# Performance work log

Hardware: AMD Instinct MI355X
Metric: run time of the kernel (lower is better)

## Reference

```python
import jax, jax.numpy as jnp
import numpy as np
from math import sqrt

B, T, C = 4, 2048, 2048
H = 16
D = C // H  # head_dim = 128


def setup_inputs() -> dict:
    key = jax.random.key(0)
    ks = jax.random.split(key, 7)
    s = 1.0 / sqrt(C)
    return {
        "querys": jax.random.normal(ks[0], (B, T, C), dtype=jnp.float32),
        "keys": jax.random.normal(ks[1], (B, T, C), dtype=jnp.float32),
        "values": jax.random.normal(ks[2], (B, T, C), dtype=jnp.float32),
        "Wq": jax.random.normal(ks[3], (C, C), dtype=jnp.float32) * s,
        "bq": jnp.zeros((C,), dtype=jnp.float32),
        "Wk": jax.random.normal(ks[4], (C, C), dtype=jnp.float32) * s,
        "bk": jnp.zeros((C,), dtype=jnp.float32),
        "Wv": jax.random.normal(ks[5], (C, C), dtype=jnp.float32) * s,
        "bv": jnp.zeros((C,), dtype=jnp.float32),
        "Wo": jax.random.normal(ks[6], (C, C), dtype=jnp.float32) * s,
        "bo": jnp.zeros((C,), dtype=jnp.float32),
        "is_causal": 1,
    }


def reference(querys, keys, values, Wq, bq, Wk, bk, Wv, bv, Wo, bo, is_causal):
    # Linear projections: x @ W^T + b (torch nn.Linear convention), here W stored as [C_in, C_out]
    q = (querys @ Wq + bq).reshape(B, T, H, D)
    k = (keys @ Wk + bk).reshape(B, T, H, D)
    v = (values @ Wv + bv).reshape(B, T, H, D)
    # scores: [B, H, T, T]
    scores = jnp.einsum("bqhd,bkhd->bhqk", q, k) / sqrt(D)
    if is_causal:
        mask = jnp.tril(jnp.ones((T, T), dtype=bool))  # allowed positions
        scores = jnp.where(mask, scores, -jnp.inf)
    weights = jax.nn.softmax(scores, axis=-1)
    attn = jnp.einsum("bhqk,bkhd->bqhd", weights, v).reshape(B, T, C)
    return attn @ Wo + bo
```

## Files before the change

kernel.cpp:

```cpp
#include <hip/hip_runtime.h>
#include <hip/hip_bf16.h>
#include <stdint.h>

#define BB 4
#define TT 2048
#define CC 2048
#define HH 16
#define DD 128
#define MM (BB*TT)

typedef __attribute__((ext_vector_type(8))) short bh8;
typedef __attribute__((ext_vector_type(4))) float fx4;

__device__ inline ushort f2bf(float x) {
    union { float f; uint32_t u; } c; c.f = x;
    uint32_t lsb = (c.u >> 16) & 1u;
    return (ushort)((c.u + 0x7fffu + lsb) >> 16);
}

__device__ inline void async16(const void* g, void* l) {
    __builtin_amdgcn_global_load_lds(
        (const __attribute__((address_space(1))) uint32_t*)g,
        (__attribute__((address_space(3))) uint32_t*)l, 16, 0, 0);
}

__global__ __launch_bounds__(256) void convert3_k(
    const float* __restrict__ i0, const float* __restrict__ i1,
    const float* __restrict__ i2,
    ushort* __restrict__ o0, ushort* __restrict__ o1, ushort* __restrict__ o2,
    int n)
{
    const float* in; ushort* out;
    switch (blockIdx.y) {
        case 0:  in = i0; out = o0; break;
        case 1:  in = i1; out = o1; break;
        default: in = i2; out = o2; break;
    }
    int i = (int)(blockIdx.x * 256 + threadIdx.x) * 4;
    if (i + 3 < n) {
        float4 v = *(const float4*)&in[i];
        ushort4 o;
        o.x = f2bf(v.x); o.y = f2bf(v.y); o.z = f2bf(v.z); o.w = f2bf(v.w);
        *(ushort4*)&out[i] = o;
    }
}

__global__ __launch_bounds__(256) void transpose4_w_k(
    const float* __restrict__ w0, const float* __restrict__ w1,
    const float* __restrict__ w2, const float* __restrict__ w3,
    ushort* __restrict__ t0, ushort* __restrict__ t1,
    ushort* __restrict__ t2, ushort* __restrict__ t3)
{
    const float* W; ushort* Wt;
    switch (blockIdx.z) {
        case 0:  W = w0; Wt = t0; break;
        case 1:  W = w1; Wt = t1; break;
        case 2:  W = w2; Wt = t2; break;
        default: W = w3; Wt = t3; break;
    }
    __shared__ __align__(16) ushort tile[32][33];
    const int n0 = blockIdx.x * 32, k0 = blockIdx.y * 32;
    const int tx = threadIdx.x, ty = threadIdx.y;
#pragma unroll
    for (int r = 0; r < 32; r += 8)
        tile[ty + r][tx] = f2bf(W[(size_t)(k0 + ty + r) * CC + n0 + tx]);
    __syncthreads();
    const int tid = ty * 32 + tx;
    const int p = tid & 15;
    const int row = tid >> 4;
#pragma unroll
    for (int rr = 0; rr < 2; ++rr) {
        const int n_row = row + rr * 16;
        ushort2 w2;
        w2.x = tile[2 * p][n_row];
        w2.y = tile[2 * p + 1][n_row];
        *(ushort2*)&Wt[(size_t)(n0 + n_row) * CC + k0 + 2 * p] = w2;
    }
}

__global__ __launch_bounds__(256) void transpose_v_k(
    const ushort* __restrict__ V, ushort* __restrict__ Vt)
{
    __shared__ __align__(16) ushort tile[32][33];
    const int bh = blockIdx.z;
    const int b = bh >> 4, h = bh & 15;
    const int t0 = blockIdx.y * 32, d0 = blockIdx.x * 32;
    const int tx = threadIdx.x, ty = threadIdx.y;
    const ushort* Vp = V + (size_t)b * TT * CC + h * DD;
#pragma unroll
    for (int r = 0; r < 32; r += 8)
        tile[ty + r][tx] = Vp[(size_t)(t0 + ty + r) * CC + d0 + tx];
    __syncthreads();
    ushort* Vtp = Vt + (size_t)bh * DD * TT;
    const int tt = t0 + tx;
    const int pnew = (tt & ~31) | (((tt >> 2) & 3) << 3) | (((tt >> 4) & 1) << 2) | (tt & 3);
#pragma unroll
    for (int r = 0; r < 32; r += 8)
        Vtp[(size_t)(d0 + ty + r) * TT + pnew] = tile[tx][ty + r];
}

template<int OUTF>
__global__ __launch_bounds__(512, 2) void gemm_bf16_k(
    const ushort* __restrict__ A, const ushort* __restrict__ Bt,
    const float* __restrict__ bias, void* __restrict__ Cv, float osc)
{
    __shared__ __align__(16) char Gsm[2][65536];

    const int tid = (int)threadIdx.x;
    const int lane = tid & 63, wave = tid >> 6;
    const int fr = lane & 15, fg = lane >> 4;
    const int wm = wave >> 2, wn = wave & 3;

    const int n_tile = (int)blockIdx.x & 7;
    const int m_tile = (int)blockIdx.x >> 3;
    const int m0 = m_tile * 256, n0 = n_tile * 256;

    const ushort* Ag = A  + (size_t)m0 * CC;
    const ushort* Bg = Bt + (size_t)n0 * CC;
    const int nt = CC / 64;

    auto STAGE_G = [&](int t, int g) {
        if (t >= nt) return;
        const int khalf = g >> 1, isB = g & 1;
        char* base = Gsm[t & 1] + isB * 32768 + khalf * 16384;
        const ushort* src = isB ? Bg : Ag;
        const int kbase = t * 64 + khalf * 32;
#pragma unroll
        for (int l = 0; l < 2; ++l) {
            const int u = l * 512 + tid;
            const int j = u >> 3, s = u & 7;
            const int ek = s ^ (j & 7);
            const int e = (ek >> 2) & 1, ks = ek & 3;
            async16(src + (size_t)(2 * j + e) * CC + kbase + ks * 8,
                    base + u * 16);
        }
    };

    const int slot = ((((fr & 1) << 2) | fg) ^ ((fr >> 1) & 7));
    const int offA = (wm * 64 + (fr >> 1)) * 128 + slot * 16;
    const int offB = 32768 + (wn * 32 + (fr >> 1)) * 128 + slot * 16;

    fx4 acc[8][4];
#pragma unroll
    for (int i = 0; i < 8; ++i)
#pragma unroll
        for (int j = 0; j < 4; ++j)
            acc[i][j] = (fx4){0.f, 0.f, 0.f, 0.f};

#pragma unroll
    for (int g = 0; g < 4; ++g) STAGE_G(0, g);

#pragma unroll 1
    for (int t = 0; t < nt; ++t) {
        const char* kb = Gsm[t & 1];
#pragma unroll
        for (int kk = 0; kk < 2; ++kk) {
            if (t == nt - 1 && kk == 1) {
                asm volatile("s_waitcnt vmcnt(0)" ::: "memory");
            } else {
                asm volatile("s_waitcnt vmcnt(4)" ::: "memory");
            }
            __builtin_amdgcn_sched_barrier(0);
            __builtin_amdgcn_s_barrier();
            __builtin_amdgcn_sched_barrier(0);

            const char* ka = kb + kk * 16384;
            const char* kbB = kb + kk * 16384;
            bh8 afr[4], bfr[4];

#pragma unroll
            for (int nf = 0; nf < 4; ++nf)
                bfr[nf] = *(const bh8*)(kbB + offB + nf * 1024);
#pragma unroll
            for (int i = 0; i < 4; ++i)
                afr[i] = *(const bh8*)(ka + offA + i * 1024);
            STAGE_G(t + 1, kk * 2);

            __builtin_amdgcn_sched_barrier(0);
            __builtin_amdgcn_s_barrier();
            __builtin_amdgcn_sched_barrier(0);

            __builtin_amdgcn_s_setprio(1);
#pragma unroll
            for (int i = 0; i < 4; ++i)
#pragma unroll
                for (int nf = 0; nf < 4; ++nf)
                    acc[i][nf] = __builtin_amdgcn_mfma_f32_16x16x32_bf16(
                        afr[i], bfr[nf], acc[i][nf], 0, 0, 0);
            __builtin_amdgcn_s_setprio(0);

#pragma unroll
            for (int i = 0; i < 4; ++i)
                afr[i] = *(const bh8*)(ka + offA + (4 + i) * 1024);
            STAGE_G(t + 1, kk * 2 + 1);

            __builtin_amdgcn_sched_barrier(0);
            __builtin_amdgcn_s_barrier();
            __builtin_amdgcn_sched_barrier(0);

            __builtin_amdgcn_s_setprio(1);
#pragma unroll
            for (int i = 0; i < 4; ++i)
#pragma unroll
                for (int nf = 0; nf < 4; ++nf)
                    acc[4 + i][nf] = __builtin_amdgcn_mfma_f32_16x16x32_bf16(
                        afr[i], bfr[nf], acc[4 + i][nf], 0, 0, 0);
            __builtin_amdgcn_s_setprio(0);
        }
    }

#pragma unroll
    for (int nf = 0; nf < 4; ++nf) {
        const int col = n0 + wn * 64 + nf * 16 + fr;
        const float bv = bias[col];
#pragma unroll
        for (int mf = 0; mf < 8; ++mf) {
            const int row = m0 + wm * 128 + mf * 16 + fg * 4;
#pragma unroll
            for (int r = 0; r < 4; ++r) {
                float v = (acc[mf][nf][r] + bv) * osc;
                if (OUTF)
                    ((float*)Cv)[(size_t)(row + r) * CC + col] = v;
                else
                    ((ushort*)Cv)[(size_t)(row + r) * CC + col] = f2bf(v);
            }
        }
    }
}

__global__ __launch_bounds__(512, 4) void flash_attn_k(
    const ushort* __restrict__ Qm, const ushort* __restrict__ Km,
    const ushort* __restrict__ Vt, ushort* __restrict__ Om,
    const int* __restrict__ causal_p)
{
    __shared__ __align__(16) char Ksm[2][16384];
    __shared__ __align__(16) char Vsm[2][16384];

    const int tid = (int)threadIdx.x;
    const int lane = tid & 63, wave = tid >> 6;
    const int fr = lane & 15, fg = lane >> 4;
    const int causal = causal_p[0];

    const int d_raw = (int)blockIdx.x + 8 * ((int)blockIdx.y + 16 * (int)blockIdx.z);
    const int xcd = d_raw & 7, jj = d_raw >> 3;
    const int head_lin = xcd * 8 + (jj & 7);
    const int pi = jj >> 3;
    const int h = head_lin & 15, b = head_lin >> 4;

    const ushort* Qp = Qm + (size_t)b * TT * CC + h * DD;
    const ushort* Kp = Km + (size_t)b * TT * CC + h * DD;
    const ushort* Vp = Vt + (size_t)(b * HH + h) * DD * TT;
    ushort* Op = Om + (size_t)b * TT * CC + h * DD;

    auto STAGE = [&](int ti, int buf) {
        const int kv0 = ti * 64;
        {
            const int r0 = tid >> 4, s0 = tid & 15;
            async16(Kp + (size_t)(kv0 + r0) * CC + (s0 ^ (r0 & 15)) * 8,
                    Ksm[buf] + tid * 16);
            async16(Kp + (size_t)(kv0 + 32 + r0) * CC + (s0 ^ (r0 & 15)) * 8,
                    Ksm[buf] + 8192 + tid * 16);
        }
        {
            const int d0 = tid >> 3, s0 = tid & 7;
            async16(Vp + (size_t)d0 * TT + kv0 + (s0 ^ (d0 & 7)) * 8,
                    Vsm[buf] + tid * 16);
            async16(Vp + (size_t)(64 + d0) * TT + kv0 + (s0 ^ (d0 & 7)) * 8,
                    Vsm[buf] + 8192 + tid * 16);
        }
    };

#pragma unroll 1
    for (int pp = 0; pp < 2; ++pp) {
        const int tile = pp ? (15 - pi) : pi;
        const int q0 = tile * 128;
        const int qbase = q0 + wave * 16;
        const int q_idx = qbase + fr;

        bh8 qf[4];
#pragma unroll
        for (int s = 0; s < 4; ++s)
            qf[s] = *(const bh8*)&Qp[(size_t)(qbase + fr) * CC + s * 32 + fg * 8];

        fx4 o[8];
#pragma unroll
        for (int jn = 0; jn < 8; ++jn) o[jn] = (fx4){0.f, 0.f, 0.f, 0.f};
        float l_acc = 0.f;

        const int nfull  = causal ? (q0 >> 6) : (TT / 64);
        const int ntiles = causal ? (nfull + 2) : (TT / 64);

        STAGE(0, 0);
#pragma unroll 1
        for (int t = 0; t < ntiles; ++t) {
            const bool last = (t == ntiles - 1);
            if (!last) STAGE(t + 1, (t + 1) & 1);
            if (!last) { asm volatile("s_waitcnt vmcnt(4)" ::: "memory"); }
            else       { asm volatile("s_waitcnt vmcnt(0)" ::: "memory"); }
            __builtin_amdgcn_sched_barrier(0);
            __builtin_amdgcn_s_barrier();
            __builtin_amdgcn_sched_barrier(0);

            const int kv0 = t * 64;
            const char* kb = Ksm[t & 1];
            const char* vb = Vsm[t & 1];
            const bool domask = causal && (t >= nfull);
            const bool active = !domask || (kv0 <= qbase + 15);

            if (active) {
                fx4 s4[4];
#pragma unroll
                for (int j = 0; j < 4; ++j) s4[j] = (fx4){0.f, 0.f, 0.f, 0.f};
                __builtin_amdgcn_s_setprio(1);
#pragma unroll
                for (int st = 0; st < 4; ++st) {
                    bh8 kf[4];
#pragma unroll
                    for (int j = 0; j < 4; ++j)
                        kf[j] = *(const bh8*)(kb + (j * 16 + fr) * 256 +
                                              ((st * 64 + fg * 16) ^ (fr << 4)));
#pragma unroll
                    for (int j = 0; j < 4; ++j)
                        s4[j] = __builtin_amdgcn_mfma_f32_16x16x32_bf16(
                            kf[j], qf[st], s4[j], 0, 0, 0);
                }
                __builtin_amdgcn_s_setprio(0);

#pragma unroll
                for (int g = 0; g < 2; ++g) {
                    float pg[2][4];
#pragma unroll
                    for (int j2 = 0; j2 < 2; ++j2) {
                        const int jb = g * 2 + j2;
#pragma unroll
                        for (int r = 0; r < 4; ++r) {
                            float v = s4[jb][r];
                            if (domask && (kv0 + jb * 16 + fg * 4 + r > q_idx))
                                v = -1e30f;
                            pg[j2][r] = exp2f(v);
                        }
                        l_acc += (pg[j2][0] + pg[j2][1]) + (pg[j2][2] + pg[j2][3]);
                    }
                    union { uint u[4]; bh8 h; } pk;
                    asm("v_cvt_pk_bf16_f32 %0, %1, %2"
                        : "=v"(pk.u[0]) : "v"(pg[0][0]), "v"(pg[0][1]));
                    asm("v_cvt_pk_bf16_f32 %0, %1, %2"
                        : "=v"(pk.u[1]) : "v"(pg[0][2]), "v"(pg[0][3]));
                    asm("v_cvt_pk_bf16_f32 %0, %1, %2"
                        : "=v"(pk.u[2]) : "v"(pg[1][0]), "v"(pg[1][1]));
                    asm("v_cvt_pk_bf16_f32 %0, %1, %2"
                        : "=v"(pk.u[3]) : "v"(pg[1][2]), "v"(pg[1][3]));
                    const bh8 pf = pk.h;

                    __builtin_amdgcn_s_setprio(1);
#pragma unroll
                    for (int jn = 0; jn < 8; ++jn) {
                        bh8 vf = *(const bh8*)(vb + (jn * 16 + fr) * 128 +
                                               ((g * 64 + fg * 16) ^ ((fr & 7) << 4)));
                        o[jn] = __builtin_amdgcn_mfma_f32_16x16x32_bf16(
                            pf, vf, o[jn], 0, 0, 0);
                    }
                    __builtin_amdgcn_s_setprio(0);
                }
            }

            __builtin_amdgcn_sched_barrier(0);
            __builtin_amdgcn_s_barrier();
            __builtin_amdgcn_sched_barrier(0);
        }

        float lsum = l_acc;
        lsum += __shfl_xor(lsum, 16);
        lsum += __shfl_xor(lsum, 32);

#pragma unroll
        for (int r = 0; r < 4; ++r) {
            const float inv = 1.0f / __shfl(lsum, fg * 4 + r, 16);
            const size_t rowoff = (size_t)(qbase + fg * 4 + r) * CC;
#pragma unroll
            for (int jn = 0; jn < 8; ++jn)
                Op[rowoff + jn * 16 + fr] = f2bf(o[jn][r] * inv);
        }
    }
}

extern "C" void kernel_launch(void* const* d_in, const int* in_sizes, int n_in,
                              void* d_out, int out_size, void* d_ws, size_t ws_size,
                              hipStream_t stream)
{
    (void)in_sizes; (void)n_in; (void)out_size;
    const float* querys = (const float*)d_in[0];
    const float* keys   = (const float*)d_in[1];
    const float* values = (const float*)d_in[2];
    const float* Wq = (const float*)d_in[3];
    const float* bq = (const float*)d_in[4];
    const float* Wk = (const float*)d_in[5];
    const float* bk = (const float*)d_in[6];
    const float* Wv = (const float*)d_in[7];
    const float* bv = (const float*)d_in[8];
    const float* Wo = (const float*)d_in[9];
    const float* bo = (const float*)d_in[10];
    const int* is_causal = (const int*)d_in[11];

    const size_t WBYTES = (size_t)CC * CC * 2;
    const size_t XBYTES = (size_t)MM * CC * 2;
    if (ws_size < 4 * WBYTES + 4 * XBYTES) return;

    uint8_t* ws = (uint8_t*)d_ws;
    ushort* WqT = (ushort*)(ws);
    ushort* WkT = (ushort*)(ws + WBYTES);
    ushort* WvT = (ushort*)(ws + 2 * WBYTES);
    ushort* WoT = (ushort*)(ws + 3 * WBYTES);
    uint8_t* act = ws + 4 * WBYTES;
    ushort* Xq = (ushort*)(act);
    ushort* Xk = (ushort*)(act + XBYTES);
    ushort* Xv = (ushort*)(act + 2 * XBYTES);
    ushort* Qb = (ushort*)(act + 3 * XBYTES);
    ushort* Kb = Xq;
    ushort* Vb = Xk;
    ushort* Vt = Xv;
    ushort* Ob = Xk;

    dim3 tb(32, 8);
    transpose4_w_k<<<dim3(CC / 32, CC / 32, 4), tb, 0, stream>>>(
        Wq, Wk, Wv, Wo, WqT, WkT, WvT, WoT);

    const int nX = MM * CC;
    convert3_k<<<dim3(nX / 4 / 256, 3), 256, 0, stream>>>(
        querys, keys, values, Xq, Xk, Xv, nX);

    dim3 gg((MM / 256) * (CC / 256));

    const float QSC = 0.12751789836306614f;

    gemm_bf16_k<0><<<gg, 512, 0, stream>>>(Xq, WqT, bq, Qb, QSC);
    gemm_bf16_k<0><<<gg, 512, 0, stream>>>(Xk, WkT, bk, Kb, 1.0f);
    gemm_bf16_k<0><<<gg, 512, 0, stream>>>(Xv, WvT, bv, Vb, 1.0f);

    dim3 gvt(DD / 32, TT / 32, BB * HH);
    transpose_v_k<<<gvt, tb, 0, stream>>>(Vb, Vt);

    dim3 ga(8, HH, BB);
    flash_attn_k<<<ga, 512, 0, stream>>>(Qb, Kb, Vt, Ob, is_causal);

    gemm_bf16_k<1><<<gg, 512, 0, stream>>>(Ob, WoT, bo, d_out, 1.0f);
}
```

Before: 509.1 us.

## Give each attention wave two query blocks and compute row sums with MFMA

The flash attention kernel now runs 4 waves per block, and each wave handles 32 query rows as two 16-row blocks. Every K and V fragment read from LDS therefore feeds twice as many MFMAs, which halves LDS traffic per unit of work. The softmax denominator now comes from an MFMA of the bf16 probabilities against a vector of ones instead of scalar adds and cross-lane shuffles. In exchange, register pressure roughly doubles, occupancy drops, fewer waves share each block, and the row sum now uses the bf16-rounded probabilities.

```diff
diff --git a/kernel.cpp b/kernel.cpp
--- a/kernel.cpp
+++ b/kernel.cpp
@@ -228,7 +228,7 @@
     }
 }
 
-__global__ __launch_bounds__(512, 4) void flash_attn_k(
+__global__ __launch_bounds__(256, 2) void flash_attn_k(
     const ushort* __restrict__ Qm, const ushort* __restrict__ Km,
     const ushort* __restrict__ Vt, ushort* __restrict__ Om,
     const int* __restrict__ causal_p)
@@ -252,21 +252,24 @@
     const ushort* Vp = Vt + (size_t)(b * HH + h) * DD * TT;
     ushort* Op = Om + (size_t)b * TT * CC + h * DD;
 
+    const bh8 onesf = {0x3F80, 0x3F80, 0x3F80, 0x3F80,
+                       0x3F80, 0x3F80, 0x3F80, 0x3F80};
+
     auto STAGE = [&](int ti, int buf) {
         const int kv0 = ti * 64;
-        {
-            const int r0 = tid >> 4, s0 = tid & 15;
+#pragma unroll
+        for (int c = 0; c < 4; ++c) {
+            const int u = c * 256 + tid;
+            const int r0 = u >> 4, s0 = u & 15;
             async16(Kp + (size_t)(kv0 + r0) * CC + (s0 ^ (r0 & 15)) * 8,
-                    Ksm[buf] + tid * 16);
-            async16(Kp + (size_t)(kv0 + 32 + r0) * CC + (s0 ^ (r0 & 15)) * 8,
-                    Ksm[buf] + 8192 + tid * 16);
-        }
-        {
-            const int d0 = tid >> 3, s0 = tid & 7;
+                    Ksm[buf] + (size_t)u * 16);
+        }
+#pragma unroll
+        for (int c = 0; c < 4; ++c) {
+            const int u = c * 256 + tid;
+            const int d0 = u >> 3, s0 = u & 7;
             async16(Vp + (size_t)d0 * TT + kv0 + (s0 ^ (d0 & 7)) * 8,
-                    Vsm[buf] + tid * 16);
-            async16(Vp + (size_t)(64 + d0) * TT + kv0 + (s0 ^ (d0 & 7)) * 8,
-                    Vsm[buf] + 8192 + tid * 16);
+                    Vsm[buf] + (size_t)u * 16);
         }
     };
 
@@ -274,18 +277,24 @@
     for (int pp = 0; pp < 2; ++pp) {
         const int tile = pp ? (15 - pi) : pi;
         const int q0 = tile * 128;
-        const int qbase = q0 + wave * 16;
-        const int q_idx = qbase + fr;
-
-        bh8 qf[4];
-#pragma unroll
-        for (int s = 0; s < 4; ++s)
-            qf[s] = *(const bh8*)&Qp[(size_t)(qbase + fr) * CC + s * 32 + fg * 8];
-
-        fx4 o[8];
-#pragma unroll
-        for (int jn = 0; jn < 8; ++jn) o[jn] = (fx4){0.f, 0.f, 0.f, 0.f};
-        float l_acc = 0.f;
+        const int qbase = q0 + wave * 32;
+
+        bh8 qf[2][4];
+#pragma unroll
+        for (int qq = 0; qq < 2; ++qq)
+#pragma unroll
+            for (int s = 0; s < 4; ++s)
+                qf[qq][s] = *(const bh8*)&Qp[(size_t)(qbase + qq * 16 + fr) * CC +
+                                             s * 32 + fg * 8];
+
+        fx4 o[2][8];
+#pragma unroll
+        for (int qq = 0; qq < 2; ++qq)
+#pragma unroll
+            for (int jn = 0; jn < 8; ++jn) o[qq][jn] = (fx4){0.f, 0.f, 0.f, 0.f};
+        fx4 o_l[2];
+        o_l[0] = (fx4){0.f, 0.f, 0.f, 0.f};
+        o_l[1] = (fx4){0.f, 0.f, 0.f, 0.f};
 
         const int nfull  = causal ? (q0 >> 6) : (TT / 64);
         const int ntiles = causal ? (nfull + 2) : (TT / 64);
@@ -295,7 +304,7 @@
         for (int t = 0; t < ntiles; ++t) {
             const bool last = (t == ntiles - 1);
             if (!last) STAGE(t + 1, (t + 1) & 1);
-            if (!last) { asm volatile("s_waitcnt vmcnt(4)" ::: "memory"); }
+            if (!last) { asm volatile("s_waitcnt vmcnt(8)" ::: "memory"); }
             else       { asm volatile("s_waitcnt vmcnt(0)" ::: "memory"); }
             __builtin_amdgcn_sched_barrier(0);
             __builtin_amdgcn_s_barrier();
@@ -305,12 +314,14 @@
             const char* kb = Ksm[t & 1];
             const char* vb = Vsm[t & 1];
             const bool domask = causal && (t >= nfull);
-            const bool active = !domask || (kv0 <= qbase + 15);
+            const bool active = !domask || (kv0 <= qbase + 31);
 
             if (active) {
-                fx4 s4[4];
-#pragma unroll
-                for (int j = 0; j < 4; ++j) s4[j] = (fx4){0.f, 0.f, 0.f, 0.f};
+                fx4 s4[2][4];
+#pragma unroll
+                for (int qq = 0; qq < 2; ++qq)
+#pragma unroll
+                    for (int j = 0; j < 4; ++j) s4[qq][j] = (fx4){0.f, 0.f, 0.f, 0.f};
                 __builtin_amdgcn_s_setprio(1);
 #pragma unroll
                 for (int st = 0; st < 4; ++st) {
@@ -320,45 +331,56 @@
                         kf[j] = *(const bh8*)(kb + (j * 16 + fr) * 256 +
                                               ((st * 64 + fg * 16) ^ (fr << 4)));
 #pragma unroll
-                    for (int j = 0; j < 4; ++j)
-                        s4[j] = __builtin_amdgcn_mfma_f32_16x16x32_bf16(
-                            kf[j], qf[st], s4[j], 0, 0, 0);
+                    for (int j = 0; j < 4; ++j) {
+                        s4[0][j] = __builtin_amdgcn_mfma_f32_16x16x32_bf16(
+                            kf[j], qf[0][st], s4[0][j], 0, 0, 0);
+                        s4[1][j] = __builtin_amdgcn_mfma_f32_16x16x32_bf16(
+                            kf[j], qf[1][st], s4[1][j], 0, 0, 0);
+                    }
                 }
                 __builtin_amdgcn_s_setprio(0);
 
 #pragma unroll
                 for (int g = 0; g < 2; ++g) {
-                    float pg[2][4];
-#pragma unroll
-                    for (int j2 = 0; j2 < 2; ++j2) {
-                        const int jb = g * 2 + j2;
-#pragma unroll
-                        for (int r = 0; r < 4; ++r) {
-                            float v = s4[jb][r];
-                            if (domask && (kv0 + jb * 16 + fg * 4 + r > q_idx))
-                                v = -1e30f;
-                            pg[j2][r] = exp2f(v);
+                    bh8 pf[2];
+#pragma unroll
+                    for (int qq = 0; qq < 2; ++qq) {
+                        const int q_idx = qbase + qq * 16 + fr;
+                        float pg[2][4];
+#pragma unroll
+                        for (int j2 = 0; j2 < 2; ++j2) {
+                            const int jb = g * 2 + j2;
+#pragma unroll
+                            for (int r = 0; r < 4; ++r) {
+                                float v = s4[qq][jb][r];
+                                if (domask && (kv0 + jb * 16 + fg * 4 + r > q_idx))
+                                    v = -1e30f;
+                                pg[j2][r] = exp2f(v);
+                            }
                         }
-                        l_acc += (pg[j2][0] + pg[j2][1]) + (pg[j2][2] + pg[j2][3]);
+                        union { uint u[4]; bh8 h; } pk;
+                        asm("v_cvt_pk_bf16_f32 %0, %1, %2"
+                            : "=v"(pk.u[0]) : "v"(pg[0][0]), "v"(pg[0][1]));
+                        asm("v_cvt_pk_bf16_f32 %0, %1, %2"
+                            : "=v"(pk.u[1]) : "v"(pg[0][2]), "v"(pg[0][3]));
+                        asm("v_cvt_pk_bf16_f32 %0, %1, %2"
+                            : "=v"(pk.u[2]) : "v"(pg[1][0]), "v"(pg[1][1]));
+                        asm("v_cvt_pk_bf16_f32 %0, %1, %2"
+                            : "=v"(pk.u[3]) : "v"(pg[1][2]), "v"(pg[1][3]));
+                        pf[qq] = pk.h;
+                        o_l[qq] = __builtin_amdgcn_mfma_f32_16x16x32_bf16(
+                            pf[qq], onesf, o_l[qq], 0, 0, 0);
                     }
-                    union { uint u[4]; bh8 h; } pk;
-                    asm("v_cvt_pk_bf16_f32 %0, %1, %2"
-                        : "=v"(pk.u[0]) : "v"(pg[0][0]), "v"(pg[0][1]));
-                    asm("v_cvt_pk_bf16_f32 %0, %1, %2"
-                        : "=v"(pk.u[1]) : "v"(pg[0][2]), "v"(pg[0][3]));
-                    asm("v_cvt_pk_bf16_f32 %0, %1, %2"
-                        : "=v"(pk.u[2]) : "v"(pg[1][0]), "v"(pg[1][1]));
-                    asm("v_cvt_pk_bf16_f32 %0, %1, %2"
-                        : "=v"(pk.u[3]) : "v"(pg[1][2]), "v"(pg[1][3]));
-                    const bh8 pf = pk.h;
 
                     __builtin_amdgcn_s_setprio(1);
 #pragma unroll
                     for (int jn = 0; jn < 8; ++jn) {
                         bh8 vf = *(const bh8*)(vb + (jn * 16 + fr) * 128 +
                                                ((g * 64 + fg * 16) ^ ((fr & 7) << 4)));
-                        o[jn] = __builtin_amdgcn_mfma_f32_16x16x32_bf16(
-                            pf, vf, o[jn], 0, 0, 0);
+                        o[0][jn] = __builtin_amdgcn_mfma_f32_16x16x32_bf16(
+                            pf[0], vf, o[0][jn], 0, 0, 0);
+                        o[1][jn] = __builtin_amdgcn_mfma_f32_16x16x32_bf16(
+                            pf[1], vf, o[1][jn], 0, 0, 0);
                     }
                     __builtin_amdgcn_s_setprio(0);
                 }
@@ -369,18 +391,16 @@
             __builtin_amdgcn_sched_barrier(0);
         }
 
-        float lsum = l_acc;
-        lsum += __shfl_xor(lsum, 16);
-        lsum += __shfl_xor(lsum, 32);
-
-#pragma unroll
-        for (int r = 0; r < 4; ++r) {
-            const float inv = 1.0f / __shfl(lsum, fg * 4 + r, 16);
-            const size_t rowoff = (size_t)(qbase + fg * 4 + r) * CC;
-#pragma unroll
-            for (int jn = 0; jn < 8; ++jn)
-                Op[rowoff + jn * 16 + fr] = f2bf(o[jn][r] * inv);
-        }
+#pragma unroll
+        for (int qq = 0; qq < 2; ++qq)
+#pragma unroll
+            for (int r = 0; r < 4; ++r) {
+                const float inv = 1.0f / o_l[qq][r];
+                const size_t rowoff = (size_t)(qbase + qq * 16 + fg * 4 + r) * CC;
+#pragma unroll
+                for (int jn = 0; jn < 8; ++jn)
+                    Op[rowoff + jn * 16 + fr] = f2bf(o[qq][jn][r] * inv);
+            }
     }
 }
 
@@ -441,7 +461,7 @@
     transpose_v_k<<<gvt, tb, 0, stream>>>(Vb, Vt);
 
     dim3 ga(8, HH, BB);
-    flash_attn_k<<<ga, 512, 0, stream>>>(Qb, Kb, Vt, Ob, is_causal);
+    flash_attn_k<<<ga, 256, 0, stream>>>(Qb, Kb, Vt, Ob, is_causal);
 
     gemm_bf16_k<1><<<gg, 512, 0, stream>>>(Ob, WoT, bo, d_out, 1.0f);
 }
```

New measurement: 515.4 us. No clear change (+1.2%).
